# Kernel optimization log

Measured on AMD Instinct MI355X. Metric: run time of the kernel, lower is better.

## Reference

```python
import jax, jax.numpy as jnp
import numpy as np

B, N, A = 8, 256, 180  # batch, resolution (even), n_angles


def setup_inputs() -> dict:
    key = jax.random.key(0)
    imgs = jax.random.normal(jax.random.fold_in(key, 0), (B, N, N), dtype=jnp.float32)
    # uniformly spaced projection angles over [0, pi)
    angles = jnp.linspace(0.0, np.pi, A, endpoint=False).astype(jnp.float32)
    return {"imgs": imgs, "angles": angles}


def _radon_forward(imgs, angles):
    """Parallel-beam Radon forward projection via bilinear ray sampling.

    imgs:   [B, N, N] float image batch
    angles: [A] float projection angles (radians)
    returns sinogram [B, A, N] (detector count == resolution, unit step along ray)
    """
    n = imgs.shape[-1]
    dtype = imgs.dtype
    c = (n - 1) / 2.0  # image center in pixel coords
    s = jnp.arange(n, dtype=dtype) - c  # detector positions, centered
    t = s                                # integration steps along each ray
    cos = jnp.cos(angles)[:, None, None]  # [A,1,1]
    sin = jnp.sin(angles)[:, None, None]
    # Sample point for (angle a, detector s_i, step t_j), in pixel coordinates.
    x = s[None, :, None] * cos - t[None, None, :] * sin + c  # [A, N, N]
    y = s[None, :, None] * sin + t[None, None, :] * cos + c  # [A, N, N]

    x0 = jnp.floor(x)
    y0 = jnp.floor(y)
    wx = x - x0
    wy = y - y0
    x0i = x0.astype(jnp.int32)
    y0i = y0.astype(jnp.int32)

    def corner(xi, yi, w):
        # zero-padding outside the image: mask out-of-range samples
        inb = (xi >= 0) & (xi < n) & (yi >= 0) & (yi < n)
        xc = jnp.clip(xi, 0, n - 1)
        yc = jnp.clip(yi, 0, n - 1)
        vals = imgs[:, yc, xc]  # gather -> [B, A, N, N]
        return vals * (w * inb.astype(dtype))[None]

    acc = (corner(x0i, y0i, (1.0 - wx) * (1.0 - wy))
           + corner(x0i + 1, y0i, wx * (1.0 - wy))
           + corner(x0i, y0i + 1, (1.0 - wx) * wy)
           + corner(x0i + 1, y0i + 1, wx * wy))
    return acc.sum(axis=-1)  # line integral along t -> [B, A, N]


def reference(imgs, angles):
    return _radon_forward(imgs, angles)
```

## Files before the change

### kernel.cpp

```cpp
#include <hip/hip_runtime.h>
#include <hip/hip_fp16.h>

#define NREZ 256
#define NB 8
#define NA 180

#define LW 49
#define LHMAX 46
#define MAGIC 2675u
#define CHUNK_T 32
#define NCHUNK (NREZ / CHUNK_T)

__device__ __forceinline__ __half2 bc_h2(unsigned int v) {
    return __builtin_bit_cast(__half2, v);
}

__global__ __launch_bounds__(256) void build_fp16(const float* __restrict__ img,
                                                  uint4* __restrict__ inter) {
    const int p = blockIdx.x * 256 + threadIdx.x;
    unsigned short h[NB];
#pragma unroll
    for (int b = 0; b < NB; ++b)
        h[b] = __half_as_ushort(__float2half_rn(img[b * (NREZ * NREZ) + p]));
    uint4 v;
    v.x = (unsigned)h[0] | ((unsigned)h[1] << 16);
    v.y = (unsigned)h[2] | ((unsigned)h[3] << 16);
    v.z = (unsigned)h[4] | ((unsigned)h[5] << 16);
    v.w = (unsigned)h[6] | ((unsigned)h[7] << 16);
    inter[p] = v;
}

__global__ __launch_bounds__(256) void radon_lds(const uint4* __restrict__ img,
                                                 const float* __restrict__ angles,
                                                 float* __restrict__ out) {
    __shared__ uint4 tile[LW * LHMAX];

    const int a = blockIdx.x;
    const int tid = threadIdx.x;
    const int wave = tid >> 6;
    const int lane = tid & 63;
    const int s_sub = lane & 7;
    const int t_sub = lane >> 3;
    const int sIdx = blockIdx.y * 32 + wave * 8 + s_sub;

    const float C = 127.5f;
    float sn, cs;
    sincosf(angles[a], &sn, &cs);
    const float s = (float)sIdx - C;
    const float xs = fmaf(s, cs, C);
    const float ys = fmaf(s, sn, C);

    const float s_lo = (float)(blockIdx.y * 32) - C;
    const float s_hi = s_lo + 31.f;
    const float xsl = fmaf(s_lo, cs, C), xsh = fmaf(s_hi, cs, C);
    const float ysl = fmaf(s_lo, sn, C), ysh = fmaf(s_hi, sn, C);

    float accf[NB];
#pragma unroll
    for (int b = 0; b < NB; ++b) accf[b] = 0.f;
    const __half2 hz = __float2half2_rn(0.f);

    for (int ck = 0; ck < NCHUNK; ++ck) {
        const float t_lo = (float)(ck * CHUNK_T) - C;
        const float t_hi = t_lo + 31.f;
        const float x00 = fmaf(t_lo, -sn, xsl), x01 = fmaf(t_hi, -sn, xsl);
        const float x10 = fmaf(t_lo, -sn, xsh), x11 = fmaf(t_hi, -sn, xsh);
        const float y00 = fmaf(t_lo, cs, ysl), y01 = fmaf(t_hi, cs, ysl);
        const float y10 = fmaf(t_lo, cs, ysh), y11 = fmaf(t_hi, cs, ysh);
        const int bx = (int)floorf(fminf(fminf(x00, x01), fminf(x10, x11)));
        const int by = (int)floorf(fminf(fminf(y00, y01), fminf(y10, y11)));
        int H = (int)floorf(fmaxf(fmaxf(y00, y01), fmaxf(y10, y11))) - by + 2;
        if (H > LHMAX) H = LHMAX;
        const int nslots = LW * H;

#pragma unroll
        for (int k = 0; k < 9; ++k) {
            const int slot = tid + (k << 8);
            if (slot < nslots) {
                const int r = (int)(((unsigned)slot * MAGIC) >> 17);
                const int col = slot - r * LW;
                const int gx = bx + col, gy = by + r;
                uint4 v = make_uint4(0u, 0u, 0u, 0u);
                if (gx >= 0 && gx < NREZ && gy >= 0 && gy < NREZ)
                    v = img[(gy << 8) + gx];
                tile[slot] = v;
            }
        }
        __syncthreads();

        __half2 acc01 = hz, acc23 = hz, acc45 = hz, acc67 = hz;
#pragma unroll
        for (int it = 0; it < 4; ++it) {
            const float tt = t_lo + (float)(t_sub + 8 * it);
            const float x = fmaf(tt, -sn, xs);
            const float y = fmaf(tt, cs, ys);
            const float xf = floorf(x), yf = floorf(y);
            const float wu = x - xf, wv = y - yf;
            const float au = 1.f - wu, av = 1.f - wv;
            const __half2 w00 = __float2half2_rn(au * av);
            const __half2 w10 = __float2half2_rn(wu * av);
            const __half2 w01 = __float2half2_rn(au * wv);
            const __half2 w11 = __float2half2_rn(wu * wv);
            const int u0 = (int)xf - bx;
            const int v0 = (int)yf - by;
            const int base = v0 * LW + u0;
            const uint4 p00 = tile[base];
            const uint4 p10 = tile[base + 1];
            const uint4 p01 = tile[base + LW];
            const uint4 p11 = tile[base + LW + 1];
            acc01 = __hfma2(w00, bc_h2(p00.x), acc01);
            acc01 = __hfma2(w10, bc_h2(p10.x), acc01);
            acc01 = __hfma2(w01, bc_h2(p01.x), acc01);
            acc01 = __hfma2(w11, bc_h2(p11.x), acc01);
            acc23 = __hfma2(w00, bc_h2(p00.y), acc23);
            acc23 = __hfma2(w10, bc_h2(p10.y), acc23);
            acc23 = __hfma2(w01, bc_h2(p01.y), acc23);
            acc23 = __hfma2(w11, bc_h2(p11.y), acc23);
            acc45 = __hfma2(w00, bc_h2(p00.z), acc45);
            acc45 = __hfma2(w10, bc_h2(p10.z), acc45);
            acc45 = __hfma2(w01, bc_h2(p01.z), acc45);
            acc45 = __hfma2(w11, bc_h2(p11.z), acc45);
            acc67 = __hfma2(w00, bc_h2(p00.w), acc67);
            acc67 = __hfma2(w10, bc_h2(p10.w), acc67);
            acc67 = __hfma2(w01, bc_h2(p01.w), acc67);
            acc67 = __hfma2(w11, bc_h2(p11.w), acc67);
        }
        accf[0] += __low2float(acc01); accf[1] += __high2float(acc01);
        accf[2] += __low2float(acc23); accf[3] += __high2float(acc23);
        accf[4] += __low2float(acc45); accf[5] += __high2float(acc45);
        accf[6] += __low2float(acc67); accf[7] += __high2float(acc67);
        __syncthreads();
    }

#pragma unroll
    for (int b = 0; b < NB; ++b) {
        float v = accf[b];
        v += __shfl_xor(v, 8);
        v += __shfl_xor(v, 16);
        v += __shfl_xor(v, 32);
        accf[b] = v;
    }
    if (t_sub == 0) {
#pragma unroll
        for (int b = 0; b < NB; ++b) {
            out[(b * NA + a) * NREZ + sIdx] = accf[b];
        }
    }
}

__global__ __launch_bounds__(256) void radon_plain(const float* __restrict__ img,
                                                   const float* __restrict__ angles,
                                                   float* __restrict__ out) {
    const int a = blockIdx.x;
    const int tid = threadIdx.x;
    const int wave = tid >> 6;
    const int lane = tid & 63;
    const int s_sub = lane & 7;
    const int t_sub = lane >> 3;
    const int sIdx = blockIdx.y * 32 + wave * 8 + s_sub;
    const float c = 127.5f;
    float sn, cs;
    sincosf(angles[a], &sn, &cs);
    const float s = (float)sIdx - c;
    float acc[NB];
#pragma unroll
    for (int b = 0; b < NB; ++b) acc[b] = 0.f;
    for (int j = 0; j < NREZ / 8; ++j) {
        const float tt = (float)(t_sub + 8 * j) - c;
        const float x = s * cs - tt * sn + c;
        const float y = s * sn + tt * cs + c;
        const float xf = floorf(x), yf = floorf(y);
        const int u0 = (int)xf, v0 = (int)yf;
        if (u0 < -1 || u0 >= NREZ || v0 < -1 || v0 >= NREZ) continue;
        const float wu = x - xf, wv = y - yf;
        const bool iu0 = (u0 >= 0), iu1 = (u0 + 1 <= NREZ - 1);
        const bool iv0 = (v0 >= 0), iv1 = (v0 + 1 <= NREZ - 1);
        const float w00 = (1.f - wu) * (1.f - wv) * ((iu0 && iv0) ? 1.f : 0.f);
        const float w10 = wu * (1.f - wv) * ((iu1 && iv0) ? 1.f : 0.f);
        const float w01 = (1.f - wu) * wv * ((iu0 && iv1) ? 1.f : 0.f);
        const float w11 = wu * wv * ((iu1 && iv1) ? 1.f : 0.f);
        const int u0c = min(max(u0, 0), NREZ - 1);
        const int u1c = min(u0 + 1, NREZ - 1);
        const int v0c = min(max(v0, 0), NREZ - 1);
        const int v1c = min(v0 + 1, NREZ - 1);
#pragma unroll
        for (int b = 0; b < NB; ++b) {
            const float* p = img + b * (NREZ * NREZ);
            acc[b] += w00 * p[v0c * NREZ + u0c] + w10 * p[v0c * NREZ + u1c] +
                      w01 * p[v1c * NREZ + u0c] + w11 * p[v1c * NREZ + u1c];
        }
    }
#pragma unroll
    for (int b = 0; b < NB; ++b) {
        float v = acc[b];
        v += __shfl_xor(v, 8);
        v += __shfl_xor(v, 16);
        v += __shfl_xor(v, 32);
        acc[b] = v;
    }
    if (t_sub == 0) {
#pragma unroll
        for (int b = 0; b < NB; ++b) out[(b * NA + a) * NREZ + sIdx] = acc[b];
    }
}

extern "C" void kernel_launch(void* const* d_in, const int* in_sizes, int n_in,
                              void* d_out, int out_size, void* d_ws, size_t ws_size,
                              hipStream_t stream) {
    (void)in_sizes; (void)n_in; (void)out_size;
    const float* imgs = (const float*)d_in[0];
    const float* angles = (const float*)d_in[1];
    float* out = (float*)d_out;

    const size_t need = (size_t)NREZ * NREZ * 16;
    dim3 grid(NA, NREZ / 32);
    if (ws_size >= need) {
        uint4* inter = (uint4*)d_ws;
        build_fp16<<<NREZ * NREZ / 256, 256, 0, stream>>>(imgs, inter);
        radon_lds<<<grid, 256, 0, stream>>>(inter, angles, out);
    } else {
        radon_plain<<<grid, 256, 0, stream>>>(imgs, angles, out);
    }
}
```

Baseline: 103.3 us.

## Prefetch next chunk's image tile into registers while computing current chunk

Each chunk's bilinear-sampling compute now overlaps with global loads for the next chunk's bounding-box tile, which are held in registers and written to LDS after a barrier. The tile fill also changes from a magic-divide slot mapping to one row per wave iteration with 48 lanes, and the LDS row stride is padded to 51. This aims to hide global-load latency behind LDS-bound compute. In exchange, each thread holds 12 uint4 prefetch registers, which raises VGPR pressure and may lower occupancy.

```diff
diff --git a/kernel.cpp b/kernel.cpp
--- a/kernel.cpp
+++ b/kernel.cpp
@@ -5,11 +5,11 @@
 #define NB 8
 #define NA 180
 
-#define LW 49
-#define LHMAX 46
-#define MAGIC 2675u
+#define LW 51
+#define LH 46
 #define CHUNK_T 32
 #define NCHUNK (NREZ / CHUNK_T)
+#define RPW 12
 
 __device__ __forceinline__ __half2 bc_h2(unsigned int v) {
     return __builtin_bit_cast(__half2, v);
@@ -33,7 +33,7 @@
 __global__ __launch_bounds__(256) void radon_lds(const uint4* __restrict__ img,
                                                  const float* __restrict__ angles,
                                                  float* __restrict__ out) {
-    __shared__ uint4 tile[LW * LHMAX];
+    __shared__ uint4 tile[LW * LH];
 
     const int a = blockIdx.x;
     const int tid = threadIdx.x;
@@ -55,39 +55,58 @@
     const float xsl = fmaf(s_lo, cs, C), xsh = fmaf(s_hi, cs, C);
     const float ysl = fmaf(s_lo, sn, C), ysh = fmaf(s_hi, sn, C);
 
-    float accf[NB];
-#pragma unroll
-    for (int b = 0; b < NB; ++b) accf[b] = 0.f;
-    const __half2 hz = __float2half2_rn(0.f);
-
-    for (int ck = 0; ck < NCHUNK; ++ck) {
+    auto bbox = [&](int ck, int& bx, int& by, int& H) {
         const float t_lo = (float)(ck * CHUNK_T) - C;
         const float t_hi = t_lo + 31.f;
         const float x00 = fmaf(t_lo, -sn, xsl), x01 = fmaf(t_hi, -sn, xsl);
         const float x10 = fmaf(t_lo, -sn, xsh), x11 = fmaf(t_hi, -sn, xsh);
         const float y00 = fmaf(t_lo, cs, ysl), y01 = fmaf(t_hi, cs, ysl);
         const float y10 = fmaf(t_lo, cs, ysh), y11 = fmaf(t_hi, cs, ysh);
-        const int bx = (int)floorf(fminf(fminf(x00, x01), fminf(x10, x11)));
-        const int by = (int)floorf(fminf(fminf(y00, y01), fminf(y10, y11)));
-        int H = (int)floorf(fmaxf(fmaxf(y00, y01), fmaxf(y10, y11))) - by + 2;
-        if (H > LHMAX) H = LHMAX;
-        const int nslots = LW * H;
-
-#pragma unroll
-        for (int k = 0; k < 9; ++k) {
-            const int slot = tid + (k << 8);
-            if (slot < nslots) {
-                const int r = (int)(((unsigned)slot * MAGIC) >> 17);
-                const int col = slot - r * LW;
-                const int gx = bx + col, gy = by + r;
-                uint4 v = make_uint4(0u, 0u, 0u, 0u);
-                if (gx >= 0 && gx < NREZ && gy >= 0 && gy < NREZ)
-                    v = img[(gy << 8) + gx];
-                tile[slot] = v;
+        bx = (int)floorf(fminf(fminf(x00, x01), fminf(x10, x11)));
+        by = (int)floorf(fminf(fminf(y00, y01), fminf(y10, y11)));
+        int h = (int)floorf(fmaxf(fmaxf(y00, y01), fmaxf(y10, y11))) - by + 2;
+        H = (h > LH) ? LH : h;
+    };
+
+    float accf[NB];
+#pragma unroll
+    for (int b = 0; b < NB; ++b) accf[b] = 0.f;
+    const __half2 hz = __float2half2_rn(0.f);
+
+    int bx, by, H;
+    bbox(0, bx, by, H);
+#pragma unroll
+    for (int k = 0; k < RPW; ++k) {
+        const int row = wave + 4 * k;
+        if (row < H && lane < 48) {
+            const int gx = bx + lane, gy = by + row;
+            uint4 v = make_uint4(0u, 0u, 0u, 0u);
+            if (gx >= 0 && gx < NREZ && gy >= 0 && gy < NREZ)
+                v = img[(gy << 8) + gx];
+            tile[row * LW + lane] = v;
+        }
+    }
+
+    for (int ck = 0; ck < NCHUNK; ++ck) {
+        __syncthreads();
+
+        int nbx = 0, nby = 0, nH = 0;
+        uint4 pf[RPW];
+        if (ck + 1 < NCHUNK) {
+            bbox(ck + 1, nbx, nby, nH);
+#pragma unroll
+            for (int k = 0; k < RPW; ++k) {
+                const int row = wave + 4 * k;
+                pf[k] = make_uint4(0u, 0u, 0u, 0u);
+                if (row < nH && lane < 48) {
+                    const int gx = nbx + lane, gy = nby + row;
+                    if (gx >= 0 && gx < NREZ && gy >= 0 && gy < NREZ)
+                        pf[k] = img[(gy << 8) + gx];
+                }
             }
         }
-        __syncthreads();
-
+
+        const float t_lo = (float)(ck * CHUNK_T) - C;
         __half2 acc01 = hz, acc23 = hz, acc45 = hz, acc67 = hz;
 #pragma unroll
         for (int it = 0; it < 4; ++it) {
@@ -101,9 +120,9 @@
             const __half2 w10 = __float2half2_rn(wu * av);
             const __half2 w01 = __float2half2_rn(au * wv);
             const __half2 w11 = __float2half2_rn(wu * wv);
-            const int u0 = (int)xf - bx;
-            const int v0 = (int)yf - by;
-            const int base = v0 * LW + u0;
+            const int c = (int)xf - bx;
+            const int r = (int)yf - by;
+            const int base = r * LW + c;
             const uint4 p00 = tile[base];
             const uint4 p10 = tile[base + 1];
             const uint4 p01 = tile[base + LW];
@@ -129,7 +148,17 @@
         accf[2] += __low2float(acc23); accf[3] += __high2float(acc23);
         accf[4] += __low2float(acc45); accf[5] += __high2float(acc45);
         accf[6] += __low2float(acc67); accf[7] += __high2float(acc67);
+
         __syncthreads();
+
+        if (ck + 1 < NCHUNK) {
+#pragma unroll
+            for (int k = 0; k < RPW; ++k) {
+                const int row = wave + 4 * k;
+                if (row < nH && lane < 48) tile[row * LW + lane] = pf[k];
+            }
+            bx = nbx; by = nby;
+        }
     }
 
 #pragma unroll
```

Result: no change. 101.5 us (-1.7%).

## Stage image tiles into LDS with direct global-to-LDS loads from padded buffer

Applied to the files above, without the earlier changes.

The packed fp16 image is now written into a zero-padded 258x258 global buffer, cleared with a memset each call. That padding lets each wave copy whole 64-element rows straight into LDS with global_load_lds, with no per-slot bounds checks or the magic-number division. Rows are placed at a small per-row offset from a lookup table, intended to spread LDS bank conflicts. Adds an extra memset launch, wider fixed-size loads, and a per-sample out-of-range test in the inner loop.

```diff
diff --git a/kernel.cpp b/kernel.cpp
--- a/kernel.cpp
+++ b/kernel.cpp
@@ -5,9 +5,12 @@
 #define NB 8
 #define NA 180
 
-#define LW 49
-#define LHMAX 46
-#define MAGIC 2675u
+#define GW 258
+#define GBYTES ((size_t)GW * GW * 16)
+
+#define LW 72
+#define LH 46
+#define QTAB 0x64317520u
 #define CHUNK_T 32
 #define NCHUNK (NREZ / CHUNK_T)
 
@@ -15,9 +18,16 @@
     return __builtin_bit_cast(__half2, v);
 }
 
-__global__ __launch_bounds__(256) void build_fp16(const float* __restrict__ img,
-                                                  uint4* __restrict__ inter) {
+__device__ __forceinline__ void dma16(const uint4* g, uint4* l) {
+    __builtin_amdgcn_global_load_lds(
+        (const __attribute__((address_space(1))) void*)g,
+        (__attribute__((address_space(3))) void*)l, 16, 0, 0);
+}
+
+__global__ __launch_bounds__(256) void build_fp16g(const float* __restrict__ img,
+                                                   uint4* __restrict__ gbuf) {
     const int p = blockIdx.x * 256 + threadIdx.x;
+    const int y = p >> 8, x = p & 255;
     unsigned short h[NB];
 #pragma unroll
     for (int b = 0; b < NB; ++b)
@@ -27,13 +37,13 @@
     v.y = (unsigned)h[2] | ((unsigned)h[3] << 16);
     v.z = (unsigned)h[4] | ((unsigned)h[5] << 16);
     v.w = (unsigned)h[6] | ((unsigned)h[7] << 16);
-    inter[p] = v;
-}
-
-__global__ __launch_bounds__(256) void radon_lds(const uint4* __restrict__ img,
+    gbuf[(size_t)(y + 1) * GW + (x + 1)] = v;
+}
+
+__global__ __launch_bounds__(256) void radon_dma(const uint4* __restrict__ gbuf,
                                                  const float* __restrict__ angles,
                                                  float* __restrict__ out) {
-    __shared__ uint4 tile[LW * LHMAX];
+    __shared__ uint4 tile[LW * LH];
 
     const int a = blockIdx.x;
     const int tid = threadIdx.x;
@@ -55,12 +65,7 @@
     const float xsl = fmaf(s_lo, cs, C), xsh = fmaf(s_hi, cs, C);
     const float ysl = fmaf(s_lo, sn, C), ysh = fmaf(s_hi, sn, C);
 
-    float accf[NB];
-#pragma unroll
-    for (int b = 0; b < NB; ++b) accf[b] = 0.f;
-    const __half2 hz = __float2half2_rn(0.f);
-
-    for (int ck = 0; ck < NCHUNK; ++ck) {
+    auto window = [&](int ck, int& bxs, int& bys) {
         const float t_lo = (float)(ck * CHUNK_T) - C;
         const float t_hi = t_lo + 31.f;
         const float x00 = fmaf(t_lo, -sn, xsl), x01 = fmaf(t_hi, -sn, xsl);
@@ -69,25 +74,38 @@
         const float y10 = fmaf(t_lo, cs, ysh), y11 = fmaf(t_hi, cs, ysh);
         const int bx = (int)floorf(fminf(fminf(x00, x01), fminf(x10, x11)));
         const int by = (int)floorf(fminf(fminf(y00, y01), fminf(y10, y11)));
-        int H = (int)floorf(fmaxf(fmaxf(y00, y01), fmaxf(y10, y11))) - by + 2;
-        if (H > LHMAX) H = LHMAX;
-        const int nslots = LW * H;
-
-#pragma unroll
-        for (int k = 0; k < 9; ++k) {
-            const int slot = tid + (k << 8);
-            if (slot < nslots) {
-                const int r = (int)(((unsigned)slot * MAGIC) >> 17);
-                const int col = slot - r * LW;
-                const int gx = bx + col, gy = by + r;
-                uint4 v = make_uint4(0u, 0u, 0u, 0u);
-                if (gx >= 0 && gx < NREZ && gy >= 0 && gy < NREZ)
-                    v = img[(gy << 8) + gx];
-                tile[slot] = v;
+        bxs = min(max(bx, -1), 193);
+        bys = min(max(by, -1), 212);
+    };
+
+    auto stage = [&](int bxs, int bys) {
+#pragma unroll
+        for (int k = 0; k < 12; ++k) {
+            const int row = wave + 4 * k;
+            if (row < LH) {
+                const int gy = bys + row;
+                if (gy <= 256) {
+                    const unsigned qr = (QTAB >> ((row & 7) << 2)) & 7u;
+                    const uint4* gp = gbuf + (size_t)(gy + 1) * GW + (bxs + 1) + lane;
+                    dma16(gp, &tile[row * LW + qr]);
+                }
             }
         }
+    };
+
+    float accf[NB];
+#pragma unroll
+    for (int b = 0; b < NB; ++b) accf[b] = 0.f;
+    const __half2 hz = __float2half2_rn(0.f);
+
+    int bxs, bys;
+    window(0, bxs, bys);
+    stage(bxs, bys);
+
+    for (int ck = 0; ck < NCHUNK; ++ck) {
         __syncthreads();
 
+        const float t_lo = (float)(ck * CHUNK_T) - C;
         __half2 acc01 = hz, acc23 = hz, acc45 = hz, acc67 = hz;
 #pragma unroll
         for (int it = 0; it < 4; ++it) {
@@ -95,41 +113,53 @@
             const float x = fmaf(tt, -sn, xs);
             const float y = fmaf(tt, cs, ys);
             const float xf = floorf(x), yf = floorf(y);
-            const float wu = x - xf, wv = y - yf;
-            const float au = 1.f - wu, av = 1.f - wv;
-            const __half2 w00 = __float2half2_rn(au * av);
-            const __half2 w10 = __float2half2_rn(wu * av);
-            const __half2 w01 = __float2half2_rn(au * wv);
-            const __half2 w11 = __float2half2_rn(wu * wv);
-            const int u0 = (int)xf - bx;
-            const int v0 = (int)yf - by;
-            const int base = v0 * LW + u0;
-            const uint4 p00 = tile[base];
-            const uint4 p10 = tile[base + 1];
-            const uint4 p01 = tile[base + LW];
-            const uint4 p11 = tile[base + LW + 1];
-            acc01 = __hfma2(w00, bc_h2(p00.x), acc01);
-            acc01 = __hfma2(w10, bc_h2(p10.x), acc01);
-            acc01 = __hfma2(w01, bc_h2(p01.x), acc01);
-            acc01 = __hfma2(w11, bc_h2(p11.x), acc01);
-            acc23 = __hfma2(w00, bc_h2(p00.y), acc23);
-            acc23 = __hfma2(w10, bc_h2(p10.y), acc23);
-            acc23 = __hfma2(w01, bc_h2(p01.y), acc23);
-            acc23 = __hfma2(w11, bc_h2(p11.y), acc23);
-            acc45 = __hfma2(w00, bc_h2(p00.z), acc45);
-            acc45 = __hfma2(w10, bc_h2(p10.z), acc45);
-            acc45 = __hfma2(w01, bc_h2(p01.z), acc45);
-            acc45 = __hfma2(w11, bc_h2(p11.z), acc45);
-            acc67 = __hfma2(w00, bc_h2(p00.w), acc67);
-            acc67 = __hfma2(w10, bc_h2(p10.w), acc67);
-            acc67 = __hfma2(w01, bc_h2(p01.w), acc67);
-            acc67 = __hfma2(w11, bc_h2(p11.w), acc67);
+            const int u0 = (int)xf, v0 = (int)yf;
+            if (u0 >= -1 && u0 <= 255 && v0 >= -1 && v0 <= 255) {
+                const float wu = x - xf, wv = y - yf;
+                const float au = 1.f - wu, av = 1.f - wv;
+                const __half2 w00 = __float2half2_rn(au * av);
+                const __half2 w10 = __float2half2_rn(wu * av);
+                const __half2 w01 = __float2half2_rn(au * wv);
+                const __half2 w11 = __float2half2_rn(wu * wv);
+                const int dx = u0 - bxs;
+                const int r = v0 - bys;
+                const unsigned qr0 = (QTAB >> ((r & 7) << 2)) & 7u;
+                const unsigned qr1 = (QTAB >> (((r + 1) & 7) << 2)) & 7u;
+                const int b00 = r * LW + (int)qr0 + dx;
+                const int b10 = (r + 1) * LW + (int)qr1 + dx;
+                const uint4 p00 = tile[b00];
+                const uint4 p10 = tile[b00 + 1];
+                const uint4 p01 = tile[b10];
+                const uint4 p11 = tile[b10 + 1];
+                acc01 = __hfma2(w00, bc_h2(p00.x), acc01);
+                acc01 = __hfma2(w10, bc_h2(p10.x), acc01);
+                acc01 = __hfma2(w01, bc_h2(p01.x), acc01);
+                acc01 = __hfma2(w11, bc_h2(p11.x), acc01);
+                acc23 = __hfma2(w00, bc_h2(p00.y), acc23);
+                acc23 = __hfma2(w10, bc_h2(p10.y), acc23);
+                acc23 = __hfma2(w01, bc_h2(p01.y), acc23);
+                acc23 = __hfma2(w11, bc_h2(p11.y), acc23);
+                acc45 = __hfma2(w00, bc_h2(p00.z), acc45);
+                acc45 = __hfma2(w10, bc_h2(p10.z), acc45);
+                acc45 = __hfma2(w01, bc_h2(p01.z), acc45);
+                acc45 = __hfma2(w11, bc_h2(p11.z), acc45);
+                acc67 = __hfma2(w00, bc_h2(p00.w), acc67);
+                acc67 = __hfma2(w10, bc_h2(p10.w), acc67);
+                acc67 = __hfma2(w01, bc_h2(p01.w), acc67);
+                acc67 = __hfma2(w11, bc_h2(p11.w), acc67);
+            }
         }
         accf[0] += __low2float(acc01); accf[1] += __high2float(acc01);
         accf[2] += __low2float(acc23); accf[3] += __high2float(acc23);
         accf[4] += __low2float(acc45); accf[5] += __high2float(acc45);
         accf[6] += __low2float(acc67); accf[7] += __high2float(acc67);
+
         __syncthreads();
+
+        if (ck + 1 < NCHUNK) {
+            window(ck + 1, bxs, bys);
+            stage(bxs, bys);
+        }
     }
 
 #pragma unroll
@@ -212,12 +242,12 @@
     const float* angles = (const float*)d_in[1];
     float* out = (float*)d_out;
 
-    const size_t need = (size_t)NREZ * NREZ * 16;
     dim3 grid(NA, NREZ / 32);
-    if (ws_size >= need) {
-        uint4* inter = (uint4*)d_ws;
-        build_fp16<<<NREZ * NREZ / 256, 256, 0, stream>>>(imgs, inter);
-        radon_lds<<<grid, 256, 0, stream>>>(inter, angles, out);
+    if (ws_size >= GBYTES) {
+        uint4* gbuf = (uint4*)d_ws;
+        hipMemsetAsync(gbuf, 0, GBYTES, stream);
+        build_fp16g<<<NREZ * NREZ / 256, 256, 0, stream>>>(imgs, gbuf);
+        radon_dma<<<grid, 256, 0, stream>>>(gbuf, angles, out);
     } else {
         radon_plain<<<grid, 256, 0, stream>>>(imgs, angles, out);
     }
```

Result: faster. 95.41 us (-7.6%).
